# Kernel optimization log

Hardware: AMD Instinct MI355X
Metric: run time of the kernel (lower is better)

The kernel has to match this reference:

```python
import jax, jax.numpy as jnp
import numpy as np

B, T, C = 4, 2048, 1024
N_HEADS = 16
HEAD_DIM = C // N_HEADS


def setup_inputs() -> dict:
    key = jax.random.key(0)
    k1, k2, k3, k4, k5 = jax.random.split(key, 5)
    x = jax.random.normal(k1, (B, T, C), dtype=jnp.float32)
    # torch Linear: y = x @ W.T + b; store W as [out, in]
    w_qkv = jax.random.normal(k2, (3 * C, C), dtype=jnp.float32) * (1.0 / np.sqrt(C))
    b_qkv = jax.random.normal(k3, (3 * C,), dtype=jnp.float32) * 0.01
    w_proj = jax.random.normal(k4, (C, C), dtype=jnp.float32) * (1.0 / np.sqrt(C))
    b_proj = jax.random.normal(k5, (C,), dtype=jnp.float32) * 0.01
    return {"x": x, "w_qkv": w_qkv, "b_qkv": b_qkv, "w_proj": w_proj, "b_proj": b_proj}


def reference(x, w_qkv, b_qkv, w_proj, b_proj):
    Bx, Tx, Cx = x.shape
    scale = 1.0 / np.sqrt(HEAD_DIM)
    qkv = x @ w_qkv.T + b_qkv                              # [B,T,3C]
    qkv = qkv.reshape(Bx, Tx, 3, N_HEADS, HEAD_DIM)
    qkv = jnp.transpose(qkv, (2, 0, 3, 1, 4))              # [3,B,H,T,D]
    q, k, v = qkv[0], qkv[1], qkv[2]
    att = jnp.einsum('bhqd,bhkd->bhqk', q, k) * scale      # [B,H,T,T]
    causal = jnp.tril(jnp.ones((Tx, Tx), dtype=bool))
    att = jnp.where(causal[None, None, :, :], att, -jnp.inf)
    att = jax.nn.softmax(att, axis=-1)
    # dropout p=0.0 (eval) -> identity
    out = jnp.einsum('bhqk,bhkd->bhqd', att, v)            # [B,H,T,D]
    out = jnp.transpose(out, (0, 2, 1, 3)).reshape(Bx, Tx, Cx)
    return out @ w_proj.T + b_proj
```

## Files before the change

kernel.cpp:

```cpp
#include <hip/hip_runtime.h>
#include <hip/hip_bf16.h>
#include <cstdint>

typedef __attribute__((ext_vector_type(8))) short bf16x8;
typedef __attribute__((ext_vector_type(4))) float f32x4;
typedef __attribute__((ext_vector_type(16))) float f32x16;

#define MFMA16(a, b, c) __builtin_amdgcn_mfma_f32_16x16x32_bf16(a, b, c, 0, 0, 0)
#define MFMA32(a, b, c) __builtin_amdgcn_mfma_f32_32x32x16_bf16(a, b, c, 0, 0, 0)

typedef __attribute__((address_space(1))) uint32_t as1_u32;
typedef __attribute__((address_space(3))) uint32_t as3_u32;
static __device__ __forceinline__ void gload16(const void* g, void* l) {
  __builtin_amdgcn_global_load_lds((as1_u32*)g, (as3_u32*)l, 16, 0, 0);
}

static __device__ __forceinline__ ushort f2b(float f) {
  union { float f; uint32_t u; } v; v.f = f;
  uint32_t u = v.u;
  uint32_t r = (u + 0x7FFFu + ((u >> 16) & 1u)) >> 16;
  return (ushort)r;
}

static __device__ __forceinline__ uint32_t cvtpk(float a, float b) {
  uint32_t r;
  asm("v_cvt_pk_bf16_f32 %0, %1, %2" : "=v"(r) : "v"(a), "v"(b));
  return r;
}
static __device__ __forceinline__ void plswap(uint32_t& a, uint32_t& b) {
  asm volatile("v_permlane32_swap_b32 %0, %1" : "+v"(a), "+v"(b));
}

#define QSCALE 0.1803368782f

#define LOFF(r, kc4) (((r) >> 1) * 64 + ((((((r) & 1) << 2) | (kc4)) ^ (((r) >> 1) & 7)) * 8))

__global__ void cvt_f32_bf16(const float* __restrict__ in, ushort* __restrict__ out, int n4) {
  int i = blockIdx.x * blockDim.x + threadIdx.x;
  if (i >= n4) return;
  const float4 v = ((const float4*)in)[i];
  ushort4 o;
  o.x = f2b(v.x); o.y = f2b(v.y); o.z = f2b(v.z); o.w = f2b(v.w);
  ((ushort4*)out)[i] = o;
}

__global__ __launch_bounds__(512, 2) void gemm_qkv_8ph(
    const ushort* __restrict__ A,
    const ushort* __restrict__ W,
    const float* __restrict__ bias,
    int M, int N, int K,
    ushort* __restrict__ q_ws, ushort* __restrict__ k_ws, ushort* __restrict__ v_ws) {
  __shared__ ushort As[2][2][2][64 * 64];
  __shared__ ushort Bs[2][2][2][64 * 64];
  const int tid = threadIdx.x;
  const int nbx = N >> 8;
  const int cpx = gridDim.x >> 3;
  const int wg = (blockIdx.x & 7) * cpx + (blockIdx.x >> 3);
  const int m0 = (wg / nbx) * 256, n0 = (wg % nbx) * 256;
  const int wid = tid >> 6, lane = tid & 63;
  const int wr = wid >> 2, wc = wid & 3;
  const int lr = lane & 15, lg = lane >> 4;
  const int prow = tid >> 3, pchk = tid & 7;
  const int lchk = pchk ^ (prow & 7);
  const int srow = prow * 2 + (lchk >> 2);
  const int skc = (lchk & 3) * 8;

  f32x4 acc[8][4] = {};
  const int nt = K >> 6;

#define STA(db_, half_, kt_)                                                  \
  { const ushort* src = A + (size_t)(m0 + (half_)*128 + srow) * K + (kt_)*64 + skc; \
    gload16(src, &As[db_][half_][0][tid * 8]);                                \
    gload16(src + 32, &As[db_][half_][1][tid * 8]); }
#define STB(db_, half_, kt_)                                                  \
  { const ushort* src = W + (size_t)(n0 + (half_)*128 + srow) * K + (kt_)*64 + skc; \
    gload16(src, &Bs[db_][half_][0][tid * 8]);                                \
    gload16(src + 32, &Bs[db_][half_][1][tid * 8]); }

  STB(0, 0, 0); STB(0, 1, 0);
  STA(0, 0, 0); STA(0, 1, 0);
  STB(1, 0, 1); STB(1, 1, 1);
  asm volatile("s_waitcnt vmcnt(4)" ::: "memory");
  __builtin_amdgcn_s_barrier();

  for (int T = 0; T < nt; ++T) {
    const int db = T & 1;
    const ushort* A0 = &As[db][wr][0][0];
    const ushort* A1 = &As[db][wr][1][0];
    const ushort* B0 = &Bs[db][wc >> 1][0][0];
    const ushort* B1 = &Bs[db][wc >> 1][1][0];
    const int brow = (wc & 1) * 64;
    bf16x8 b[4][2];
#pragma unroll
    for (int q = 0; q < 4; ++q) {
      bf16x8 a[2][2];
#pragma unroll
      for (int mm = 0; mm < 2; ++mm) {
        const int r = (2 * q + mm) * 16 + lr;
        a[mm][0] = *(const bf16x8*)&A0[LOFF(r, lg)];
        a[mm][1] = *(const bf16x8*)&A1[LOFF(r, lg)];
      }
      if (q == 0) {
#pragma unroll
        for (int nf = 0; nf < 4; ++nf) {
          const int r = brow + nf * 16 + lr;
          b[nf][0] = *(const bf16x8*)&B0[LOFF(r, lg)];
          b[nf][1] = *(const bf16x8*)&B1[LOFF(r, lg)];
        }
      }
      if (q == 0) {
        if (T + 1 < nt) { STA((T + 1) & 1, 0, T + 1); STA((T + 1) & 1, 1, T + 1); }
      } else if (q == 1) {
        if (T + 2 < nt) STB(T & 1, 0, T + 2);
      } else if (q == 2) {
        if (T + 2 < nt) STB(T & 1, 1, T + 2);
      }
      __builtin_amdgcn_sched_barrier(0);
      __builtin_amdgcn_s_barrier();
      asm volatile("s_waitcnt lgkmcnt(0)" ::: "memory");
      __builtin_amdgcn_sched_barrier(0);
      __builtin_amdgcn_s_setprio(1);
#pragma unroll
      for (int kk = 0; kk < 2; ++kk)
#pragma unroll
        for (int mm = 0; mm < 2; ++mm)
#pragma unroll
          for (int nf = 0; nf < 4; ++nf)
            acc[2 * q + mm][nf] = MFMA16(a[mm][kk], b[nf][kk], acc[2 * q + mm][nf]);
      __builtin_amdgcn_s_setprio(0);
      if (q == 3) {
        if (T + 1 < nt) {
          if (T + 2 < nt)
            asm volatile("s_waitcnt vmcnt(4)" ::: "memory");
          else
            asm volatile("s_waitcnt vmcnt(0)" ::: "memory");
          __builtin_amdgcn_s_barrier();
        }
      } else {
        __builtin_amdgcn_s_barrier();
      }
    }
  }
#undef STA
#undef STB

#pragma unroll
  for (int mf = 0; mf < 8; ++mf) {
#pragma unroll
    for (int nf = 0; nf < 4; ++nf) {
      const int rowb = m0 + wr * 128 + mf * 16 + lg * 4;
      const int col = n0 + wc * 64 + nf * 16 + lr;
      float v[4];
#pragma unroll
      for (int i = 0; i < 4; ++i) v[i] = acc[mf][nf][i] + bias[col];
      const int sel = col >> 10;
      const int rem = col & 1023;
      const int h = rem >> 6, d = rem & 63;
      const int bb = rowb >> 11, t0 = rowb & 2047;
      if (sel == 2) {
        ushort4 st;
        st.x = f2b(v[0]); st.y = f2b(v[1]); st.z = f2b(v[2]); st.w = f2b(v[3]);
        *(ushort4*)&v_ws[((size_t)(bb * 16 + h) * 64 + d) * 2048 + t0] = st;
      } else if (sel == 0) {
#pragma unroll
        for (int i = 0; i < 4; ++i)
          q_ws[((size_t)(bb * 16 + h) * 2048 + t0 + i) * 64 + d] = f2b(v[i] * QSCALE);
      } else {
#pragma unroll
        for (int i = 0; i < 4; ++i)
          k_ws[((size_t)(bb * 16 + h) * 2048 + t0 + i) * 64 + d] = f2b(v[i]);
      }
    }
  }
}

__global__ __launch_bounds__(256) void gemm_proj(
    const ushort* __restrict__ A,
    const ushort* __restrict__ W,
    const float* __restrict__ bias,
    int M, int N, int K,
    float* __restrict__ out) {
  __shared__ ushort As[3][64 * 64];
  __shared__ ushort Bs[3][64 * 64];
  const int tid = threadIdx.x;
  const int nbx = N >> 7;
  const int cpx = gridDim.x >> 3;
  const int wg = (blockIdx.x & 7) * cpx + (blockIdx.x >> 3);
  const int m0 = (wg / nbx) * 128, n0 = (wg % nbx) * 128;
  const int lane = tid & 63, w = tid >> 6;
  const int lr = lane & 15, lg = lane >> 4;
  const int wm = (w >> 1) * 64, wn = (w & 1) * 64;
  f32x4 acc[4][4] = {};

  const int nt = K >> 5;

#define GSTAGE(buf_, kt_)                                                   \
  do {                                                                      \
    const ushort* Asrc = A + (size_t)m0 * K + (kt_) * 32;                   \
    const ushort* Bsrc = W + (size_t)n0 * K + (kt_) * 32;                   \
    _Pragma("unroll") for (int i_ = 0; i_ < 2; ++i_) {                      \
      const int ch = i_ * 256 + tid;                                        \
      const int prow = ch >> 3, pchk = ch & 7;                              \
      const int lchk = pchk ^ (prow & 7);                                   \
      const int r = prow * 2 + (lchk >> 2), kc = (lchk & 3) * 8;            \
      gload16(&Asrc[(size_t)r * K + kc], &As[buf_][ch * 8]);                \
      gload16(&Bsrc[(size_t)r * K + kc], &Bs[buf_][ch * 8]);                \
    }                                                                       \
  } while (0)

  GSTAGE(0, 0);
  GSTAGE(1, 1);
  asm volatile("s_waitcnt vmcnt(4)" ::: "memory");
  __builtin_amdgcn_s_barrier();
  asm volatile("" ::: "memory");

  int bcur = 0, bnxt = 2;
  for (int t = 0; t < nt; ++t) {
    if (t + 2 < nt) GSTAGE(bnxt, t + 2);
    const ushort* Asc = As[bcur];
    const ushort* Bsc = Bs[bcur];
    bf16x8 a[4], b[4];
#pragma unroll
    for (int mi = 0; mi < 4; ++mi) {
      const int r = wm + mi * 16 + lr;
      a[mi] = *(const bf16x8*)&Asc[LOFF(r, lg)];
    }
#pragma unroll
    for (int ni = 0; ni < 4; ++ni) {
      const int r = wn + ni * 16 + lr;
      b[ni] = *(const bf16x8*)&Bsc[LOFF(r, lg)];
    }
    __builtin_amdgcn_s_setprio(1);
#pragma unroll
    for (int mi = 0; mi < 4; ++mi)
#pragma unroll
      for (int ni = 0; ni < 4; ++ni)
        acc[mi][ni] = MFMA16(a[mi], b[ni], acc[mi][ni]);
    __builtin_amdgcn_s_setprio(0);
    if (t + 2 < nt)
      asm volatile("s_waitcnt vmcnt(4)" ::: "memory");
    else if (t + 1 < nt)
      asm volatile("s_waitcnt vmcnt(0)" ::: "memory");
    if (t + 1 < nt) {
      __builtin_amdgcn_s_barrier();
      asm volatile("" ::: "memory");
    }
    bcur = (bcur == 2) ? 0 : bcur + 1;
    bnxt = (bnxt == 2) ? 0 : bnxt + 1;
  }
#undef GSTAGE

#pragma unroll
  for (int mi = 0; mi < 4; ++mi) {
#pragma unroll
    for (int ni = 0; ni < 4; ++ni) {
      const int rowb = m0 + wm + mi * 16 + lg * 4;
      const int col = n0 + wn + ni * 16 + lr;
#pragma unroll
      for (int i = 0; i < 4; ++i)
        out[(size_t)(rowb + i) * N + col] = acc[mi][ni][i] + bias[col];
    }
  }
}

__global__ __launch_bounds__(256) void attn_v5(
    const ushort* __restrict__ Q, const ushort* __restrict__ K,
    const ushort* __restrict__ VT, ushort* __restrict__ O ) {
  const int blk = blockIdx.x;
  const int bh = blk & 63;
  const int pr = blk >> 6;
  const int tid = threadIdx.x;
  const int w = tid >> 6, lane = tid & 63;
  const int l31 = lane & 31, l5 = lane >> 5;
  const int bb = bh >> 4, h = bh & 15;
  const size_t base = (size_t)bh * 2048 * 64;
  const ushort* Qb = Q + base;
  const ushort* Kb = K + base;
  const ushort* VTb = VT + base;

  __shared__ ushort Ks[2][64 * 64];
  __shared__ ushort Vs[2][64 * 64];
  __shared__ float l_lds[4][32];

#define STAGE(buf, kt_)                                              \
  do {                                                               \
    const ushort* Kt = Kb + (size_t)(kt_) * 64 * 64;                 \
    const ushort* Vt = VTb + (kt_) * 64;                             \
    _Pragma("unroll") for (int i_ = 0; i_ < 2; ++i_) {               \
      const int ch = i_ * 256 + tid;                                 \
      const int r = ch >> 3;                                         \
      const int csw = ((ch & 7) ^ (r & 7)) * 8;                      \
      gload16(&Kt[(size_t)r * 64 + csw], &Ks[buf][ch * 8]);          \
      gload16(&Vt[(size_t)r * 2048 + csw], &Vs[buf][ch * 8]);        \
    }                                                                \
  } while (0)

#pragma unroll 1
  for (int ph = 0; ph < 2; ++ph) {
    const int s = ph ? pr : 15 - pr;
    const int q0w = s * 128 + w * 32;
    const int nt = 2 * s + 2;
    const int qlane = q0w + l31;

    bf16x8 qf[4];
#pragma unroll
    for (int dblk = 0; dblk < 4; ++dblk)
      qf[dblk] = *(const bf16x8*)&Qb[(size_t)qlane * 64 + dblk * 16 + l5 * 8];

    f32x16 o0 = {}, o1 = {};
    float lsum = 0.f;

    STAGE(0, 0);
    __syncthreads();

    for (int kt = 0; kt < nt; ++kt) {
      const int cur = kt & 1;
      if (kt + 1 < nt) STAGE(cur ^ 1, kt + 1);
      const int k0 = kt << 6;
      const ushort* Ksc = Ks[cur];
      const ushort* Vsc = Vs[cur];
#pragma unroll
      for (int kblk = 0; kblk < 2; ++kblk) {
        const int kbase = k0 + kblk * 32;
        if (kbase <= q0w + 31) {
          f32x16 st = {};
          __builtin_amdgcn_s_setprio(1);
#pragma unroll
          for (int dblk = 0; dblk < 4; ++dblk) {
            const int row = kblk * 32 + l31;
            bf16x8 ka = *(const bf16x8*)&Ksc[row * 64 + (((dblk * 2 + l5) ^ (row & 7)) * 8)];
            st = MFMA32(ka, qf[dblk], st);
          }
          __builtin_amdgcn_s_setprio(0);
          if (kbase + 31 > q0w) {
#pragma unroll
            for (int r = 0; r < 16; ++r) {
              const int kk = kbase + (r & 3) + 8 * (r >> 2) + 4 * l5;
              st[r] = (kk <= qlane) ? st[r] : -INFINITY;
            }
          }
          float p[16];
#pragma unroll
          for (int r = 0; r < 16; ++r) {
            p[r] = __builtin_amdgcn_exp2f(st[r]);
            lsum += p[r];
          }
#pragma unroll
          for (int sbl = 0; sbl < 2; ++sbl) {
            uint32_t P0 = cvtpk(p[8 * sbl + 0], p[8 * sbl + 1]);
            uint32_t P1 = cvtpk(p[8 * sbl + 2], p[8 * sbl + 3]);
            uint32_t P2 = cvtpk(p[8 * sbl + 4], p[8 * sbl + 5]);
            uint32_t P3 = cvtpk(p[8 * sbl + 6], p[8 * sbl + 7]);
            plswap(P0, P2);
            plswap(P1, P3);
            union { uint32_t u[4]; bf16x8 v; } pk;
            pk.u[0] = P0; pk.u[1] = P1; pk.u[2] = P2; pk.u[3] = P3;
            const int kchunk = kblk * 4 + sbl * 2 + l5;
            __builtin_amdgcn_s_setprio(1);
#pragma unroll
            for (int db2 = 0; db2 < 2; ++db2) {
              const int vrow = db2 * 32 + l31;
              bf16x8 vb = *(const bf16x8*)&Vsc[vrow * 64 + ((kchunk ^ (vrow & 7)) * 8)];
              if (db2 == 0) o0 = MFMA32(pk.v, vb, o0);
              else          o1 = MFMA32(pk.v, vb, o1);
            }
            __builtin_amdgcn_s_setprio(0);
          }
        }
      }
      __syncthreads();
    }

    const float lfull = lsum + __shfl_xor(lsum, 32);
    if (lane < 32) l_lds[w][lane] = 1.f / lfull;
#pragma unroll
    for (int r = 0; r < 16; ++r) {
      const int qoff = (r & 3) + 8 * (r >> 2) + 4 * l5;
      const float inv = l_lds[w][qoff];
      const int t = q0w + qoff;
      ushort* op = &O[(size_t)(bb * 2048 + t) * 1024 + h * 64 + l31];
      op[0] = f2b(o0[r] * inv);
      op[32] = f2b(o1[r] * inv);
    }
  }
#undef STAGE
}

extern "C" void kernel_launch(void* const* d_in, const int* in_sizes, int n_in,
                              void* d_out, int out_size, void* d_ws, size_t ws_size,
                              hipStream_t stream) {
  const float* x = (const float*)d_in[0];
  const float* w_qkv = (const float*)d_in[1];
  const float* b_qkv = (const float*)d_in[2];
  const float* w_proj = (const float*)d_in[3];
  const float* b_proj = (const float*)d_in[4];
  float* out = (float*)d_out;

  char* ws = (char*)d_ws;
  const size_t SZ_X = (size_t)8192 * 1024 * 2;
  const size_t SZ_WQ = (size_t)3072 * 1024 * 2;
  const size_t SZ_WP = (size_t)1024 * 1024 * 2;
  ushort* xb = (ushort*)(ws);
  ushort* wqb = (ushort*)(ws + SZ_X);
  ushort* wpb = (ushort*)(ws + SZ_X + SZ_WQ);
  ushort* q_ws = (ushort*)(ws + SZ_X + SZ_WQ + SZ_WP);
  ushort* k_ws = q_ws + (size_t)8192 * 1024;
  ushort* v_ws = k_ws + (size_t)8192 * 1024;

  cvt_f32_bf16<<<8388608 / 4 / 256, 256, 0, stream>>>(x, xb, 8388608 / 4);
  cvt_f32_bf16<<<3145728 / 4 / 256, 256, 0, stream>>>(w_qkv, wqb, 3145728 / 4);
  cvt_f32_bf16<<<1048576 / 4 / 256, 256, 0, stream>>>(w_proj, wpb, 1048576 / 4);

  gemm_qkv_8ph<<<384, 512, 0, stream>>>(
      xb, wqb, b_qkv, 8192, 3072, 1024, q_ws, k_ws, v_ws);

  attn_v5<<<512, 256, 0, stream>>>(q_ws, k_ws, v_ws, xb);

  gemm_proj<<<512, 256, 0, stream>>>(
      xb, wpb, b_proj, 8192, 1024, 1024, out);
}
```

Baseline: 174.4 us.

## Halve QKV GEMM M-tile to 128 rows and double grid to 768 blocks

The QKV projection GEMM tile shrinks from 256x256 to 128x256, giving 768 workgroups instead of 384, so more work is in flight across the 256 CUs and the tail is less uneven. The 4-phase inner loop becomes 2 phases per K-step, with A prefetch and B prefetch moved to the new phases, and the accumulator array is halved. In exchange, each tile reuses less data, so global and LDS traffic per FLOP rises, and the extra barriers per K-step now cover less MFMA work.

```diff
diff --git a/kernel.cpp b/kernel.cpp
--- a/kernel.cpp
+++ b/kernel.cpp
@@ -50,13 +50,12 @@
     const float* __restrict__ bias,
     int M, int N, int K,
     ushort* __restrict__ q_ws, ushort* __restrict__ k_ws, ushort* __restrict__ v_ws) {
-  __shared__ ushort As[2][2][2][64 * 64];
+  __shared__ ushort As[2][2][64 * 64];
   __shared__ ushort Bs[2][2][2][64 * 64];
   const int tid = threadIdx.x;
-  const int nbx = N >> 8;
   const int cpx = gridDim.x >> 3;
   const int wg = (blockIdx.x & 7) * cpx + (blockIdx.x >> 3);
-  const int m0 = (wg / nbx) * 256, n0 = (wg % nbx) * 256;
+  const int m0 = (wg / 12) * 128, n0 = (wg % 12) * 256;
   const int wid = tid >> 6, lane = tid & 63;
   const int wr = wid >> 2, wc = wid & 3;
   const int lr = lane & 15, lg = lane >> 4;
@@ -65,56 +64,47 @@
   const int srow = prow * 2 + (lchk >> 2);
   const int skc = (lchk & 3) * 8;
 
-  f32x4 acc[8][4] = {};
+  f32x4 acc[4][4] = {};
   const int nt = K >> 6;
 
-#define STA(db_, half_, kt_)                                                  \
-  { const ushort* src = A + (size_t)(m0 + (half_)*128 + srow) * K + (kt_)*64 + skc; \
-    gload16(src, &As[db_][half_][0][tid * 8]);                                \
-    gload16(src + 32, &As[db_][half_][1][tid * 8]); }
+#define STA(db_, kt_)                                                         \
+  { const ushort* src = A + (size_t)(m0 + srow) * K + (kt_)*64 + skc;         \
+    gload16(src, &As[db_][0][tid * 8]);                                       \
+    gload16(src + 32, &As[db_][1][tid * 8]); }
 #define STB(db_, half_, kt_)                                                  \
   { const ushort* src = W + (size_t)(n0 + (half_)*128 + srow) * K + (kt_)*64 + skc; \
     gload16(src, &Bs[db_][half_][0][tid * 8]);                                \
     gload16(src + 32, &Bs[db_][half_][1][tid * 8]); }
 
   STB(0, 0, 0); STB(0, 1, 0);
-  STA(0, 0, 0); STA(0, 1, 0);
+  STA(0, 0);
   STB(1, 0, 1); STB(1, 1, 1);
   asm volatile("s_waitcnt vmcnt(4)" ::: "memory");
   __builtin_amdgcn_s_barrier();
 
+  const int bhalf = wc >> 1, brow = (wc & 1) * 64;
   for (int T = 0; T < nt; ++T) {
     const int db = T & 1;
-    const ushort* A0 = &As[db][wr][0][0];
-    const ushort* A1 = &As[db][wr][1][0];
-    const ushort* B0 = &Bs[db][wc >> 1][0][0];
-    const ushort* B1 = &Bs[db][wc >> 1][1][0];
-    const int brow = (wc & 1) * 64;
+    const ushort* Asub0 = &As[db][0][0];
+    const ushort* Asub1 = &As[db][1][0];
+    const ushort* Bsub0 = &Bs[db][bhalf][0][0];
+    const ushort* Bsub1 = &Bs[db][bhalf][1][0];
     bf16x8 b[4][2];
-#pragma unroll
-    for (int q = 0; q < 4; ++q) {
+    {
       bf16x8 a[2][2];
 #pragma unroll
       for (int mm = 0; mm < 2; ++mm) {
-        const int r = (2 * q + mm) * 16 + lr;
-        a[mm][0] = *(const bf16x8*)&A0[LOFF(r, lg)];
-        a[mm][1] = *(const bf16x8*)&A1[LOFF(r, lg)];
+        const int r = wr * 64 + mm * 16 + lr;
+        a[mm][0] = *(const bf16x8*)&Asub0[LOFF(r, lg)];
+        a[mm][1] = *(const bf16x8*)&Asub1[LOFF(r, lg)];
       }
-      if (q == 0) {
-#pragma unroll
-        for (int nf = 0; nf < 4; ++nf) {
-          const int r = brow + nf * 16 + lr;
-          b[nf][0] = *(const bf16x8*)&B0[LOFF(r, lg)];
-          b[nf][1] = *(const bf16x8*)&B1[LOFF(r, lg)];
-        }
+#pragma unroll
+      for (int nf = 0; nf < 4; ++nf) {
+        const int r = brow + nf * 16 + lr;
+        b[nf][0] = *(const bf16x8*)&Bsub0[LOFF(r, lg)];
+        b[nf][1] = *(const bf16x8*)&Bsub1[LOFF(r, lg)];
       }
-      if (q == 0) {
-        if (T + 1 < nt) { STA((T + 1) & 1, 0, T + 1); STA((T + 1) & 1, 1, T + 1); }
-      } else if (q == 1) {
-        if (T + 2 < nt) STB(T & 1, 0, T + 2);
-      } else if (q == 2) {
-        if (T + 2 < nt) STB(T & 1, 1, T + 2);
-      }
+      if (T + 1 < nt) STA((T + 1) & 1, T + 1);
       __builtin_amdgcn_sched_barrier(0);
       __builtin_amdgcn_s_barrier();
       asm volatile("s_waitcnt lgkmcnt(0)" ::: "memory");
@@ -126,29 +116,47 @@
         for (int mm = 0; mm < 2; ++mm)
 #pragma unroll
           for (int nf = 0; nf < 4; ++nf)
-            acc[2 * q + mm][nf] = MFMA16(a[mm][kk], b[nf][kk], acc[2 * q + mm][nf]);
+            acc[mm][nf] = MFMA16(a[mm][kk], b[nf][kk], acc[mm][nf]);
       __builtin_amdgcn_s_setprio(0);
-      if (q == 3) {
-        if (T + 1 < nt) {
-          if (T + 2 < nt)
-            asm volatile("s_waitcnt vmcnt(4)" ::: "memory");
-          else
-            asm volatile("s_waitcnt vmcnt(0)" ::: "memory");
-          __builtin_amdgcn_s_barrier();
-        }
-      } else {
-        __builtin_amdgcn_s_barrier();
+      __builtin_amdgcn_s_barrier();
+    }
+    {
+      bf16x8 a[2][2];
+#pragma unroll
+      for (int mm = 0; mm < 2; ++mm) {
+        const int r = wr * 64 + (2 + mm) * 16 + lr;
+        a[mm][0] = *(const bf16x8*)&Asub0[LOFF(r, lg)];
+        a[mm][1] = *(const bf16x8*)&Asub1[LOFF(r, lg)];
       }
+      if (T + 2 < nt) { STB(db, 0, T + 2); STB(db, 1, T + 2); }
+      __builtin_amdgcn_sched_barrier(0);
+      __builtin_amdgcn_s_barrier();
+      asm volatile("s_waitcnt lgkmcnt(0)" ::: "memory");
+      __builtin_amdgcn_sched_barrier(0);
+      __builtin_amdgcn_s_setprio(1);
+#pragma unroll
+      for (int kk = 0; kk < 2; ++kk)
+#pragma unroll
+        for (int mm = 0; mm < 2; ++mm)
+#pragma unroll
+          for (int nf = 0; nf < 4; ++nf)
+            acc[2 + mm][nf] = MFMA16(a[mm][kk], b[nf][kk], acc[2 + mm][nf]);
+      __builtin_amdgcn_s_setprio(0);
+      if (T + 2 < nt)
+        asm volatile("s_waitcnt vmcnt(4)" ::: "memory");
+      else if (T + 1 < nt)
+        asm volatile("s_waitcnt vmcnt(0)" ::: "memory");
+      if (T + 1 < nt) __builtin_amdgcn_s_barrier();
     }
   }
 #undef STA
 #undef STB
 
 #pragma unroll
-  for (int mf = 0; mf < 8; ++mf) {
+  for (int mf = 0; mf < 4; ++mf) {
 #pragma unroll
     for (int nf = 0; nf < 4; ++nf) {
-      const int rowb = m0 + wr * 128 + mf * 16 + lg * 4;
+      const int rowb = m0 + wr * 64 + mf * 16 + lg * 4;
       const int col = n0 + wc * 64 + nf * 16 + lr;
       float v[4];
 #pragma unroll
@@ -411,7 +419,7 @@
   cvt_f32_bf16<<<3145728 / 4 / 256, 256, 0, stream>>>(w_qkv, wqb, 3145728 / 4);
   cvt_f32_bf16<<<1048576 / 4 / 256, 256, 0, stream>>>(w_proj, wpb, 1048576 / 4);
 
-  gemm_qkv_8ph<<<384, 512, 0, stream>>>(
+  gemm_qkv_8ph<<<768, 512, 0, stream>>>(
       xb, wqb, b_qkv, 8192, 3072, 1024, q_ws, k_ws, v_ws);
 
   attn_v5<<<512, 256, 0, stream>>>(q_ws, k_ws, v_ws, xb);
```

Measured after the change: 171.6 us. About the same (-1.6%).
